# Optimization experiments

Hardware: AMD Instinct MI355X
Metric: run time of the kernel (lower is better)

The kernel has to match this reference:

```python
import jax, jax.numpy as jnp
import numpy as np

NEG_INF = -1e9  # masked_fill value from the torch module


def setup_inputs() -> dict:
    key = jax.random.key(0)
    ks = jax.random.split(key, 6)
    n_edges, hidden = 100000, 256
    n_paths, max_len = 20000, 16
    edge_emb = jax.random.normal(ks[0], (n_edges, hidden), dtype=jnp.float32)
    paths = jax.random.randint(ks[1], (n_paths, max_len), 0, n_edges)
    path_lens = jax.random.randint(ks[2], (n_paths,), 0, max_len)  # +1 in reference -> 1..max_len
    path_mask = jax.random.randint(ks[3], (n_paths,), 0, 2)
    # nn.Linear(hidden, 1) parameters
    W = jax.random.normal(ks[4], (1, hidden), dtype=jnp.float32) / np.sqrt(hidden)
    b = jax.random.normal(ks[5], (1,), dtype=jnp.float32) * 0.01
    return {"edge_emb": edge_emb, "paths": paths, "path_lens": path_lens,
            "path_mask": path_mask, "W": W, "b": b, "deterministic": 1}


def reference(edge_emb, paths, path_lens, path_mask, W, b, deterministic):
    # ragged per-path mean: emulate `for p in paths: edge_emb[p].mean(0)` with padded gather
    lens = path_lens + 1                                   # [P], 1..max_len
    pos = jnp.arange(paths.shape[1])                        # [L]
    valid = pos[None, :] < lens[:, None]                    # [P, L]
    gathered = edge_emb[paths]                              # [P, L, H]
    z = jnp.sum(jnp.where(valid[..., None], gathered, 0.0), axis=1) / lens[:, None].astype(edge_emb.dtype)  # [P, H]
    logits = z @ W[0] + b[0]                                # [P]  (Linear(H,1).squeeze())
    logits = jnp.where(path_mask == 0, NEG_INF, logits)
    logp = jax.nn.log_softmax(logits)
    if deterministic:
        p = jnp.argmax(logits)
    else:
        p = jax.random.categorical(jax.random.key(42), logits)
    logprob = logp[p]
    return (p, logprob, z[p])
```

## Files before the change

kernel.cpp:

```cpp
#include <hip/hip_runtime.h>
#include <math.h>

#define NEG_INF -1e9f

__global__ __launch_bounds__(256) void k_edge_dot(
    const float* __restrict__ emb, const float* __restrict__ W,
    float* __restrict__ s, int n_edges)
{
    int wave = (blockIdx.x * (int)blockDim.x + (int)threadIdx.x) >> 6;
    int lane = threadIdx.x & 63;
    if (wave >= n_edges) return;
    const float4 e = ((const float4*)emb)[wave * 64 + lane];
    const float4 w = ((const float4*)W)[lane];
    float d = e.x * w.x + e.y * w.y + e.z * w.z + e.w * w.w;
#pragma unroll
    for (int off = 32; off; off >>= 1) d += __shfl_down(d, off, 64);
    if (lane == 0) s[wave] = d;
}

__global__ __launch_bounds__(256) void k_logits16(
    const float* __restrict__ s, const int* __restrict__ paths,
    const int* __restrict__ path_lens, const int* __restrict__ path_mask,
    const float* __restrict__ b, float* __restrict__ logits, int n_paths)
{
    int p = blockIdx.x * (int)blockDim.x + (int)threadIdx.x;
    if (p >= n_paths) return;
    int len = path_lens[p] + 1;
    const int4* pp4 = (const int4*)(paths + (size_t)p * 16);
    int4 a0 = pp4[0], a1 = pp4[1], a2 = pp4[2], a3 = pp4[3];
    int idx[16] = { a0.x, a0.y, a0.z, a0.w, a1.x, a1.y, a1.z, a1.w,
                    a2.x, a2.y, a2.z, a2.w, a3.x, a3.y, a3.z, a3.w };
    float acc = 0.f;
#pragma unroll
    for (int j = 0; j < 16; ++j) {
        float v = s[idx[j]];
        acc += (j < len) ? v : 0.f;
    }
    float logit = acc / (float)len + b[0];
    logits[p] = (path_mask[p] == 0) ? NEG_INF : logit;
}

__global__ __launch_bounds__(256) void k_logits_gen(
    const float* __restrict__ s, const int* __restrict__ paths,
    const int* __restrict__ path_lens, const int* __restrict__ path_mask,
    const float* __restrict__ b, float* __restrict__ logits,
    int n_paths, int max_len)
{
    int p = blockIdx.x * (int)blockDim.x + (int)threadIdx.x;
    if (p >= n_paths) return;
    int len = path_lens[p] + 1;
    const int* pp = paths + (size_t)p * max_len;
    float acc = 0.f;
    for (int j = 0; j < len; ++j) acc += s[pp[j]];
    logits[p] = (path_mask[p] == 0) ? NEG_INF : (acc / (float)len + b[0]);
}

__global__ __launch_bounds__(1024) void k_final(
    const float* __restrict__ logits, const float* __restrict__ emb,
    const int* __restrict__ paths, const int* __restrict__ path_lens,
    float* __restrict__ out, int n_paths, int max_len)
{
    __shared__ float sv[16];
    __shared__ int   si[16];
    __shared__ float ssum[16];
    __shared__ int   s_p, s_len;
    __shared__ float s_max, s_logprob;

    int tid = threadIdx.x, lane = tid & 63, wv = tid >> 6;
    int n4 = n_paths >> 2;
    const float4* l4 = (const float4*)logits;

    float bv = -INFINITY; int bi = 0x7fffffff;
    for (int i = tid; i < n4; i += 1024) {
        float4 v = l4[i];
        int base = i << 2;
        if (v.x > bv) { bv = v.x; bi = base; }
        if (v.y > bv) { bv = v.y; bi = base + 1; }
        if (v.z > bv) { bv = v.z; bi = base + 2; }
        if (v.w > bv) { bv = v.w; bi = base + 3; }
    }
    for (int i = (n4 << 2) + tid; i < n_paths; i += 1024) {
        float v = logits[i];
        if (v > bv) { bv = v; bi = i; }
    }
#pragma unroll
    for (int off = 32; off; off >>= 1) {
        float ov = __shfl_down(bv, off, 64);
        int   oi = __shfl_down(bi, off, 64);
        if (ov > bv || (ov == bv && oi < bi)) { bv = ov; bi = oi; }
    }
    if (lane == 0) { sv[wv] = bv; si[wv] = bi; }
    __syncthreads();
    if (tid == 0) {
        float mv = sv[0]; int mi = si[0];
        for (int w = 1; w < 16; ++w)
            if (sv[w] > mv || (sv[w] == mv && si[w] < mi)) { mv = sv[w]; mi = si[w]; }
        s_max = mv; s_p = mi; s_len = path_lens[mi] + 1;
    }
    __syncthreads();
    float mx = s_max;

    float se = 0.f;
    for (int i = tid; i < n4; i += 1024) {
        float4 v = l4[i];
        se += expf(v.x - mx) + expf(v.y - mx) + expf(v.z - mx) + expf(v.w - mx);
    }
    for (int i = (n4 << 2) + tid; i < n_paths; i += 1024)
        se += expf(logits[i] - mx);
#pragma unroll
    for (int off = 32; off; off >>= 1) se += __shfl_down(se, off, 64);
    if (lane == 0) ssum[wv] = se;
    __syncthreads();
    if (tid == 0) {
        float t = 0.f;
        for (int w = 0; w < 16; ++w) t += ssum[w];
        s_logprob = -logf(t);
    }
    __syncthreads();

    int p = s_p, len = s_len;
    if (tid < 256) {
        const int* pp = paths + (size_t)p * max_len;
        float acc = 0.f;
        for (int j = 0; j < len; ++j)
            acc += emb[(size_t)pp[j] * 256 + tid];
        out[2 + tid] = acc / (float)len;
    }
    if (tid == 0) { out[0] = (float)p; out[1] = s_logprob; }
}

extern "C" void kernel_launch(void* const* d_in, const int* in_sizes, int n_in,
                              void* d_out, int out_size, void* d_ws, size_t ws_size,
                              hipStream_t stream) {
    const float* emb       = (const float*)d_in[0];
    const int*   paths     = (const int*)  d_in[1];
    const int*   path_lens = (const int*)  d_in[2];
    const int*   path_mask = (const int*)  d_in[3];
    const float* W         = (const float*)d_in[4];
    const float* b         = (const float*)d_in[5];

    int hidden  = in_sizes[4];
    int n_edges = in_sizes[0] / hidden;
    int n_paths = in_sizes[2];
    int max_len = in_sizes[1] / n_paths;

    float* s      = (float*)d_ws;
    float* logits = s + n_edges;

    int blocks1 = (n_edges * 64 + 255) / 256;
    k_edge_dot<<<blocks1, 256, 0, stream>>>(emb, W, s, n_edges);

    int blocks2 = (n_paths + 255) / 256;
    if (max_len == 16)
        k_logits16<<<blocks2, 256, 0, stream>>>(s, paths, path_lens, path_mask,
                                                b, logits, n_paths);
    else
        k_logits_gen<<<blocks2, 256, 0, stream>>>(s, paths, path_lens, path_mask,
                                                  b, logits, n_paths, max_len);

    k_final<<<1, 1024, 0, stream>>>(logits, emb, paths, path_lens,
                                    (float*)d_out, n_paths, max_len);
}
```

Baseline: 167.5 us.

## Fuse logits and final softmax/argmax kernels via last-block atomic counter

Merges the per-path logit kernel and the single-block final reduction into one launch: each block computes its logits, then an atomic counter picks the last finishing block, which does the argmax, log-softmax and mean gather with 256 threads. Masked paths now skip gathering their indices. This removes one kernel launch and its boundary, at the cost of a reduction done by 256 threads instead of 1024, an added memset launch, and threadfence/atomic overhead.

```diff
diff --git a/kernel.cpp b/kernel.cpp
--- a/kernel.cpp
+++ b/kernel.cpp
@@ -18,60 +18,62 @@
     if (lane == 0) s[wave] = d;
 }
 
-__global__ __launch_bounds__(256) void k_logits16(
+__global__ __launch_bounds__(256) void k_logits_final(
     const float* __restrict__ s, const int* __restrict__ paths,
     const int* __restrict__ path_lens, const int* __restrict__ path_mask,
-    const float* __restrict__ b, float* __restrict__ logits, int n_paths)
-{
-    int p = blockIdx.x * (int)blockDim.x + (int)threadIdx.x;
-    if (p >= n_paths) return;
-    int len = path_lens[p] + 1;
-    const int4* pp4 = (const int4*)(paths + (size_t)p * 16);
-    int4 a0 = pp4[0], a1 = pp4[1], a2 = pp4[2], a3 = pp4[3];
-    int idx[16] = { a0.x, a0.y, a0.z, a0.w, a1.x, a1.y, a1.z, a1.w,
-                    a2.x, a2.y, a2.z, a2.w, a3.x, a3.y, a3.z, a3.w };
-    float acc = 0.f;
-#pragma unroll
-    for (int j = 0; j < 16; ++j) {
-        float v = s[idx[j]];
-        acc += (j < len) ? v : 0.f;
-    }
-    float logit = acc / (float)len + b[0];
-    logits[p] = (path_mask[p] == 0) ? NEG_INF : logit;
-}
-
-__global__ __launch_bounds__(256) void k_logits_gen(
-    const float* __restrict__ s, const int* __restrict__ paths,
-    const int* __restrict__ path_lens, const int* __restrict__ path_mask,
-    const float* __restrict__ b, float* __restrict__ logits,
-    int n_paths, int max_len)
-{
-    int p = blockIdx.x * (int)blockDim.x + (int)threadIdx.x;
-    if (p >= n_paths) return;
-    int len = path_lens[p] + 1;
-    const int* pp = paths + (size_t)p * max_len;
-    float acc = 0.f;
-    for (int j = 0; j < len; ++j) acc += s[pp[j]];
-    logits[p] = (path_mask[p] == 0) ? NEG_INF : (acc / (float)len + b[0]);
-}
-
-__global__ __launch_bounds__(1024) void k_final(
-    const float* __restrict__ logits, const float* __restrict__ emb,
-    const int* __restrict__ paths, const int* __restrict__ path_lens,
+    const float* __restrict__ b, const float* __restrict__ emb,
+    float* __restrict__ logits, int* __restrict__ counter,
     float* __restrict__ out, int n_paths, int max_len)
 {
-    __shared__ float sv[16];
-    __shared__ int   si[16];
-    __shared__ float ssum[16];
+    int tid = threadIdx.x;
+    int p = blockIdx.x * 256 + tid;
+    if (p < n_paths) {
+        if (path_mask[p] == 0) {
+            logits[p] = NEG_INF;
+        } else {
+            int len = path_lens[p] + 1;
+            const int* pp = paths + (size_t)p * max_len;
+            float acc = 0.f;
+            if (max_len == 16) {
+                const int4* pp4 = (const int4*)pp;
+                int4 a0 = pp4[0], a1 = pp4[1], a2 = pp4[2], a3 = pp4[3];
+                int idx[16] = { a0.x, a0.y, a0.z, a0.w, a1.x, a1.y, a1.z, a1.w,
+                                a2.x, a2.y, a2.z, a2.w, a3.x, a3.y, a3.z, a3.w };
+#pragma unroll
+                for (int j = 0; j < 16; ++j) {
+                    float v = s[idx[j]];
+                    acc += (j < len) ? v : 0.f;
+                }
+            } else {
+                for (int j = 0; j < len; ++j) acc += s[pp[j]];
+            }
+            logits[p] = acc / (float)len + b[0];
+        }
+    }
+
+    __shared__ int s_last;
+    __threadfence();
+    __syncthreads();
+    if (tid == 0) {
+        int prev = atomicAdd(counter, 1);
+        s_last = (prev == (int)gridDim.x - 1);
+    }
+    __syncthreads();
+    if (!s_last) return;
+    __threadfence();
+
+    __shared__ float sv[4];
+    __shared__ int   si[4];
+    __shared__ float ssum[4];
     __shared__ int   s_p, s_len;
     __shared__ float s_max, s_logprob;
 
-    int tid = threadIdx.x, lane = tid & 63, wv = tid >> 6;
+    int lane = tid & 63, wv = tid >> 6;
     int n4 = n_paths >> 2;
     const float4* l4 = (const float4*)logits;
 
     float bv = -INFINITY; int bi = 0x7fffffff;
-    for (int i = tid; i < n4; i += 1024) {
+    for (int i = tid; i < n4; i += 256) {
         float4 v = l4[i];
         int base = i << 2;
         if (v.x > bv) { bv = v.x; bi = base; }
@@ -79,7 +81,7 @@
         if (v.z > bv) { bv = v.z; bi = base + 2; }
         if (v.w > bv) { bv = v.w; bi = base + 3; }
     }
-    for (int i = (n4 << 2) + tid; i < n_paths; i += 1024) {
+    for (int i = (n4 << 2) + tid; i < n_paths; i += 256) {
         float v = logits[i];
         if (v > bv) { bv = v; bi = i; }
     }
@@ -93,7 +95,7 @@
     __syncthreads();
     if (tid == 0) {
         float mv = sv[0]; int mi = si[0];
-        for (int w = 1; w < 16; ++w)
+        for (int w = 1; w < 4; ++w)
             if (sv[w] > mv || (sv[w] == mv && si[w] < mi)) { mv = sv[w]; mi = si[w]; }
         s_max = mv; s_p = mi; s_len = path_lens[mi] + 1;
     }
@@ -101,32 +103,31 @@
     float mx = s_max;
 
     float se = 0.f;
-    for (int i = tid; i < n4; i += 1024) {
+    for (int i = tid; i < n4; i += 256) {
         float4 v = l4[i];
         se += expf(v.x - mx) + expf(v.y - mx) + expf(v.z - mx) + expf(v.w - mx);
     }
-    for (int i = (n4 << 2) + tid; i < n_paths; i += 1024)
+    for (int i = (n4 << 2) + tid; i < n_paths; i += 256)
         se += expf(logits[i] - mx);
 #pragma unroll
     for (int off = 32; off; off >>= 1) se += __shfl_down(se, off, 64);
     if (lane == 0) ssum[wv] = se;
     __syncthreads();
     if (tid == 0) {
-        float t = 0.f;
-        for (int w = 0; w < 16; ++w) t += ssum[w];
+        float t = ssum[0] + ssum[1] + ssum[2] + ssum[3];
         s_logprob = -logf(t);
     }
     __syncthreads();
 
-    int p = s_p, len = s_len;
-    if (tid < 256) {
-        const int* pp = paths + (size_t)p * max_len;
+    int p2 = s_p, len2 = s_len;
+    {
+        const int* pp = paths + (size_t)p2 * max_len;
         float acc = 0.f;
-        for (int j = 0; j < len; ++j)
+        for (int j = 0; j < len2; ++j)
             acc += emb[(size_t)pp[j] * 256 + tid];
-        out[2 + tid] = acc / (float)len;
+        out[2 + tid] = acc / (float)len2;
     }
-    if (tid == 0) { out[0] = (float)p; out[1] = s_logprob; }
+    if (tid == 0) { out[0] = (float)p2; out[1] = s_logprob; }
 }
 
 extern "C" void kernel_launch(void* const* d_in, const int* in_sizes, int n_in,
@@ -146,18 +147,15 @@
 
     float* s      = (float*)d_ws;
     float* logits = s + n_edges;
+    int*   counter = (int*)(logits + n_paths);
+
+    hipMemsetAsync(counter, 0, sizeof(int), stream);
 
     int blocks1 = (n_edges * 64 + 255) / 256;
     k_edge_dot<<<blocks1, 256, 0, stream>>>(emb, W, s, n_edges);
 
     int blocks2 = (n_paths + 255) / 256;
-    if (max_len == 16)
-        k_logits16<<<blocks2, 256, 0, stream>>>(s, paths, path_lens, path_mask,
-                                                b, logits, n_paths);
-    else
-        k_logits_gen<<<blocks2, 256, 0, stream>>>(s, paths, path_lens, path_mask,
-                                                  b, logits, n_paths, max_len);
-
-    k_final<<<1, 1024, 0, stream>>>(logits, emb, paths, path_lens,
-                                    (float*)d_out, n_paths, max_len);
+    k_logits_final<<<blocks2, 256, 0, stream>>>(s, paths, path_lens, path_mask,
+                                                b, emb, logits, counter,
+                                                (float*)d_out, n_paths, max_len);
 }
```

Result: slower. 182.4 us (+8.9%).
